# Kernel tuning notes

Hardware: AMD Instinct MI355X
Metric: run time of the kernel (lower is better)

The kernel has to match this reference:

```python
import jax, jax.numpy as jnp
import numpy as np


def setup_inputs() -> dict:
    key = jax.random.key(0)
    k1, k2, k3 = jax.random.split(key, 3)
    B, C, H, W, F, K = 8, 32, 64, 64, 64, 3
    x = jax.random.normal(k1, (B, C, H, W), dtype=jnp.float32)
    # per-weight rational (safe Pade [5/4]) coefficients: one activation per (f, a, b, c)
    num_coef = jax.random.normal(k2, (F, K, K, C, 6), dtype=jnp.float32) * 0.1
    den_coef = jax.random.normal(k3, (F, K, K, C, 4), dtype=jnp.float32) * 0.1
    return {"x": x, "num_coef": num_coef, "den_coef": den_coef}


def _rational(x, an, bd):
    """Safe Pade rational: P(x)/(1+|x*(b1+x*(b2+x*(b3+x*b4)))|).
    x: [B,H,W,K,K,C]; an: [K,K,C,6]; bd: [K,K,C,4] (broadcast over B,H,W)."""
    num = an[..., 5]
    for i in (4, 3, 2, 1, 0):  # Horner, ascending coeff order a0..a5
        num = num * x + an[..., i]
    q = bd[..., 3]
    for i in (2, 1, 0):
        q = q * x + bd[..., i]
    den = 1.0 + jnp.abs(q * x)
    return num / den


def reference(x, num_coef, den_coef):
    B, C, H, W = x.shape
    F, K = num_coef.shape[0], num_coef.shape[1]
    p = (K - 1) // 2
    xp = jnp.pad(x, ((0, 0), (0, 0), (p, p), (p, p)))  # zero pad H,W
    xp = jnp.transpose(xp, (0, 2, 3, 1))  # [B, H+2p, W+2p, C]
    # im2col patches: [B, H, W, K, K, C]
    patches = jnp.stack(
        [jnp.stack([xp[:, a:a + H, b:b + W, :] for b in range(K)], axis=3)
         for a in range(K)], axis=3)

    def per_filter(coefs):
        an, bd = coefs  # [K,K,C,6], [K,K,C,4]
        y = _rational(patches, an, bd)  # [B,H,W,K,K,C]
        return jnp.sum(y, axis=(3, 4, 5))  # [B,H,W]

    out = jax.lax.map(per_filter, (num_coef, den_coef))  # [F,B,H,W]
    return jnp.transpose(out, (1, 0, 2, 3))  # [B,F,H,W]
```

## Files before the change

### kernel.cpp

```cpp
#include <hip/hip_runtime.h>


typedef int   iv4  __attribute__((ext_vector_type(4)));
typedef short s8v  __attribute__((ext_vector_type(8)));
typedef float f16v __attribute__((ext_vector_type(16)));

#define Bb 8
#define Cc 32
#define Hh 64
#define Ww 64
#define Ff 64
#define PW 66
#define PPLANE (PW * PW)
#define NELEM  (Bb * Cc * PPLANE)
#define NTAP   288
#define ACOEF_N (NTAP * 4 * 64)

static __device__ __forceinline__ unsigned short f2bf(float f) {
    unsigned u = __builtin_bit_cast(unsigned, f);
    u += 0x7fffu + ((u >> 16) & 1u);
    return (unsigned short)(u >> 16);
}
static __device__ __forceinline__ float bf2f(unsigned short h) {
    unsigned u = ((unsigned)h) << 16;
    return __builtin_bit_cast(float, u);
}
static __device__ __forceinline__ int pack2(unsigned short a, unsigned short b) {
    return (int)((unsigned)a | ((unsigned)b << 16));
}

__global__ __launch_bounds__(256) void powers_kernel(
    const float* __restrict__ x, iv4* __restrict__ pw)
{
    int idx = (int)blockIdx.x * 256 + (int)threadIdx.x;
    int wp = idx % PW;
    int r1 = idx / PW;
    int hp = r1 % PW;
    int pl = r1 / PW;
    float v = 0.0f;
    if (hp >= 1 && hp <= Hh && wp >= 1 && wp <= Ww)
        v = x[((size_t)pl * Hh + (hp - 1)) * Ww + (wp - 1)];
    float p1 = v, p2 = v * v, p3 = p2 * v, p4 = p2 * p2, p5 = p4 * v;
    float pv[6] = {1.0f, p1, p2, p3, p4, p5};
    unsigned short hi[6], lo[6];
#pragma unroll
    for (int e = 0; e < 6; ++e) {
        hi[e] = f2bf(pv[e]);
        lo[e] = f2bf(pv[e] - bf2f(hi[e]));
    }
    iv4 r0, r1v;
    r0.x  = pack2(hi[0], hi[1]); r0.y  = pack2(hi[2], hi[3]);
    r0.z  = pack2(hi[4], hi[5]); r0.w  = pack2(lo[1], lo[2]);
    r1v.x = pack2(lo[3], lo[4]); r1v.y = pack2(lo[5], hi[1]);
    r1v.z = pack2(hi[2], hi[3]); r1v.w = pack2(hi[4], hi[5]);
    pw[idx]         = r0;
    pw[NELEM + idx] = r1v;
}

__global__ __launch_bounds__(256) void acoef_kernel(
    const float* __restrict__ ncf, const float* __restrict__ dcf,
    iv4* __restrict__ ac)
{
    int idx = (int)blockIdx.x * 256 + (int)threadIdx.x;
    int l = idx & 63, tile = (idx >> 6) & 3, t = idx >> 8;
    int m = l & 31, g = l >> 5;
    float cv[6];
    if (tile < 2) {
        int f = tile * 32 + m;
        const float* s = ncf + ((size_t)f * NTAP + t) * 6;
        cv[0] = s[0]; cv[1] = s[1]; cv[2] = s[2];
        cv[3] = s[3]; cv[4] = s[4]; cv[5] = s[5];
    } else {
        int f = (tile - 2) * 32 + m;
        const float* s = dcf + ((size_t)f * NTAP + t) * 4;
        cv[0] = 0.0f; cv[1] = s[0]; cv[2] = s[1];
        cv[3] = s[2]; cv[4] = s[3]; cv[5] = 0.0f;
    }
    unsigned short chi[6], clo[6];
#pragma unroll
    for (int e = 0; e < 6; ++e) {
        chi[e] = f2bf(cv[e]);
        clo[e] = f2bf(cv[e] - bf2f(chi[e]));
    }
    iv4 o;
    if (g == 0) {
        o.x = pack2(chi[0], chi[1]); o.y = pack2(chi[2], chi[3]);
        o.z = pack2(chi[4], chi[5]); o.w = pack2(chi[1], chi[2]);
    } else {
        o.x = pack2(chi[3], chi[4]); o.y = pack2(chi[5], clo[1]);
        o.z = pack2(clo[2], clo[3]); o.w = pack2(clo[4], clo[5]);
    }
    ac[idx] = o;
}

__global__ __launch_bounds__(256, 4) void kan_mfma_kernel(
    const iv4* __restrict__ pw, const iv4* __restrict__ ac,
    float* __restrict__ out)
{
    const int tid = threadIdx.x;
    const int l = tid & 63, v = tid >> 6, ln = l & 31, g = l >> 5;
    const int gb = (int)blockIdx.x;
    const int wh = gb & 1, h = (gb >> 1) & 63, bb = gb >> 7;
    const int w0 = wh << 5;

    __shared__ float red[4][64][33];

    f16v acc0, acc1, zf;
#pragma unroll
    for (int r = 0; r < 16; ++r) { acc0[r] = 0.0f; acc1[r] = 0.0f; zf[r] = 0.0f; }

    const iv4* __restrict__ pwg = pw + (size_t)g * NELEM;

    const int tEnd = v * 72 + 72;
    for (int t = v * 72; t < tEnd; ++t) {
        const int c = t & 31, k2 = t >> 5;
        const int dy = k2 / 3, dx = k2 - dy * 3;
        const int elem = ((bb * Cc + c) * PW + (h + dy)) * PW + (w0 + ln + dx);
        iv4 bl = pwg[elem];
        const iv4* ap = ac + (size_t)t * 256;
        iv4 A0 = ap[l], A1 = ap[64 + l], A2 = ap[128 + l], A3 = ap[192 + l];
        s8v bF = __builtin_bit_cast(s8v, bl);

        f16v D0 = __builtin_amdgcn_mfma_f32_32x32x16_bf16(
            __builtin_bit_cast(s8v, A0), bF, zf, 0, 0, 0);
        f16v D2 = __builtin_amdgcn_mfma_f32_32x32x16_bf16(
            __builtin_bit_cast(s8v, A2), bF, zf, 0, 0, 0);
#pragma unroll
        for (int r = 0; r < 16; ++r) {
            float dd = 1.0f + __builtin_fabsf(D2[r]);
            float rc = __builtin_amdgcn_rcpf(dd);
            acc0[r] = __builtin_fmaf(D0[r], rc, acc0[r]);
        }
        f16v D1 = __builtin_amdgcn_mfma_f32_32x32x16_bf16(
            __builtin_bit_cast(s8v, A1), bF, zf, 0, 0, 0);
        f16v D3 = __builtin_amdgcn_mfma_f32_32x32x16_bf16(
            __builtin_bit_cast(s8v, A3), bF, zf, 0, 0, 0);
#pragma unroll
        for (int r = 0; r < 16; ++r) {
            float dd = 1.0f + __builtin_fabsf(D3[r]);
            float rc = __builtin_amdgcn_rcpf(dd);
            acc1[r] = __builtin_fmaf(D1[r], rc, acc1[r]);
        }
    }

#pragma unroll
    for (int r = 0; r < 16; ++r) {
        red[v][l][r]      = acc0[r];
        red[v][l][16 + r] = acc1[r];
    }
    __syncthreads();

#pragma unroll
    for (int jj = 0; jj < 8; ++jj) {
        int j = v * 8 + jj;
        float s = red[0][l][j] + red[1][l][j] + red[2][l][j] + red[3][l][j];
        int tt = j >> 4, r = j & 15;
        int f = tt * 32 + (r & 3) + ((r >> 2) << 3) + ((l >> 5) << 2);
        out[(((size_t)bb * Ff + f) * Hh + h) * Ww + w0 + ln] = s;
    }
}

extern "C" void kernel_launch(void* const* d_in, const int* in_sizes, int n_in,
                              void* d_out, int out_size, void* d_ws, size_t ws_size,
                              hipStream_t stream) {
    const float* x   = (const float*)d_in[0];
    const float* ncf = (const float*)d_in[1];
    const float* dcf = (const float*)d_in[2];
    float* out = (float*)d_out;

    iv4* pw = (iv4*)d_ws;
    iv4* ac = pw + 2 * NELEM;

    powers_kernel<<<NELEM / 256, 256, 0, stream>>>(x, pw);
    acoef_kernel<<<NTAP, 256, 0, stream>>>(ncf, dcf, ac);
    kan_mfma_kernel<<<1024, 256, 0, stream>>>(pw, ac, out);
}
```

Before: 162.0 us.

## Merge prep kernels and split filter halves across 8 waves with prefetch

```diff
diff --git a/kernel.cpp b/kernel.cpp
--- a/kernel.cpp
+++ b/kernel.cpp
@@ -14,7 +14,7 @@
 #define PPLANE (PW * PW)
 #define NELEM  (Bb * Cc * PPLANE)
 #define NTAP   288
-#define ACOEF_N (NTAP * 4 * 64)
+#define PWBLK  (NELEM / 256)
 
 static __device__ __forceinline__ unsigned short f2bf(float f) {
     unsigned u = __builtin_bit_cast(unsigned, f);
@@ -29,133 +29,137 @@
     return (int)((unsigned)a | ((unsigned)b << 16));
 }
 
-__global__ __launch_bounds__(256) void powers_kernel(
-    const float* __restrict__ x, iv4* __restrict__ pw)
+__global__ __launch_bounds__(256) void prep_kernel(
+    const float* __restrict__ x,
+    const float* __restrict__ ncf, const float* __restrict__ dcf,
+    iv4* __restrict__ pw, iv4* __restrict__ ac)
 {
-    int idx = (int)blockIdx.x * 256 + (int)threadIdx.x;
-    int wp = idx % PW;
-    int r1 = idx / PW;
-    int hp = r1 % PW;
-    int pl = r1 / PW;
-    float v = 0.0f;
-    if (hp >= 1 && hp <= Hh && wp >= 1 && wp <= Ww)
-        v = x[((size_t)pl * Hh + (hp - 1)) * Ww + (wp - 1)];
-    float p1 = v, p2 = v * v, p3 = p2 * v, p4 = p2 * p2, p5 = p4 * v;
-    float pv[6] = {1.0f, p1, p2, p3, p4, p5};
-    unsigned short hi[6], lo[6];
+    if ((int)blockIdx.x < PWBLK) {
+        int idx = (int)blockIdx.x * 256 + (int)threadIdx.x;
+        int wp = idx % PW;
+        int r1 = idx / PW;
+        int hp = r1 % PW;
+        int pl = r1 / PW;
+        float v = 0.0f;
+        if (hp >= 1 && hp <= Hh && wp >= 1 && wp <= Ww)
+            v = x[((size_t)pl * Hh + (hp - 1)) * Ww + (wp - 1)];
+        float p2 = v * v, p3 = p2 * v, p4 = p2 * p2, p5 = p4 * v;
+        float pv[6] = {1.0f, v, p2, p3, p4, p5};
+        unsigned short hi[6], lo[6];
 #pragma unroll
-    for (int e = 0; e < 6; ++e) {
-        hi[e] = f2bf(pv[e]);
-        lo[e] = f2bf(pv[e] - bf2f(hi[e]));
+        for (int e = 0; e < 6; ++e) {
+            hi[e] = f2bf(pv[e]);
+            lo[e] = f2bf(pv[e] - bf2f(hi[e]));
+        }
+        iv4 r0, r1v;
+        r0.x  = pack2(hi[0], hi[1]); r0.y  = pack2(hi[2], hi[3]);
+        r0.z  = pack2(hi[4], hi[5]); r0.w  = pack2(lo[1], lo[2]);
+        r1v.x = pack2(lo[3], lo[4]); r1v.y = pack2(lo[5], hi[1]);
+        r1v.z = pack2(hi[2], hi[3]); r1v.w = pack2(hi[4], hi[5]);
+        pw[idx]         = r0;
+        pw[NELEM + idx] = r1v;
+    } else {
+        int idx = ((int)blockIdx.x - PWBLK) * 256 + (int)threadIdx.x;
+        int l = idx & 63, tile = (idx >> 6) & 3, t = idx >> 8;
+        int m = l & 31, g = l >> 5;
+        float cv[6];
+        if (tile < 2) {
+            int f = tile * 32 + m;
+            const float* s = ncf + ((size_t)f * NTAP + t) * 6;
+            cv[0] = s[0]; cv[1] = s[1]; cv[2] = s[2];
+            cv[3] = s[3]; cv[4] = s[4]; cv[5] = s[5];
+        } else {
+            int f = (tile - 2) * 32 + m;
+            const float* s = dcf + ((size_t)f * NTAP + t) * 4;
+            cv[0] = 0.0f; cv[1] = s[0]; cv[2] = s[1];
+            cv[3] = s[2]; cv[4] = s[3]; cv[5] = 0.0f;
+        }
+        unsigned short chi[6], clo[6];
+#pragma unroll
+        for (int e = 0; e < 6; ++e) {
+            chi[e] = f2bf(cv[e]);
+            clo[e] = f2bf(cv[e] - bf2f(chi[e]));
+        }
+        iv4 o;
+        if (g == 0) {
+            o.x = pack2(chi[0], chi[1]); o.y = pack2(chi[2], chi[3]);
+            o.z = pack2(chi[4], chi[5]); o.w = pack2(chi[1], chi[2]);
+        } else {
+            o.x = pack2(chi[3], chi[4]); o.y = pack2(chi[5], clo[1]);
+            o.z = pack2(clo[2], clo[3]); o.w = pack2(clo[4], clo[5]);
+        }
+        ac[idx] = o;
     }
-    iv4 r0, r1v;
-    r0.x  = pack2(hi[0], hi[1]); r0.y  = pack2(hi[2], hi[3]);
-    r0.z  = pack2(hi[4], hi[5]); r0.w  = pack2(lo[1], lo[2]);
-    r1v.x = pack2(lo[3], lo[4]); r1v.y = pack2(lo[5], hi[1]);
-    r1v.z = pack2(hi[2], hi[3]); r1v.w = pack2(hi[4], hi[5]);
-    pw[idx]         = r0;
-    pw[NELEM + idx] = r1v;
 }
 
-__global__ __launch_bounds__(256) void acoef_kernel(
-    const float* __restrict__ ncf, const float* __restrict__ dcf,
-    iv4* __restrict__ ac)
-{
-    int idx = (int)blockIdx.x * 256 + (int)threadIdx.x;
-    int l = idx & 63, tile = (idx >> 6) & 3, t = idx >> 8;
-    int m = l & 31, g = l >> 5;
-    float cv[6];
-    if (tile < 2) {
-        int f = tile * 32 + m;
-        const float* s = ncf + ((size_t)f * NTAP + t) * 6;
-        cv[0] = s[0]; cv[1] = s[1]; cv[2] = s[2];
-        cv[3] = s[3]; cv[4] = s[4]; cv[5] = s[5];
-    } else {
-        int f = (tile - 2) * 32 + m;
-        const float* s = dcf + ((size_t)f * NTAP + t) * 4;
-        cv[0] = 0.0f; cv[1] = s[0]; cv[2] = s[1];
-        cv[3] = s[2]; cv[4] = s[3]; cv[5] = 0.0f;
-    }
-    unsigned short chi[6], clo[6];
-#pragma unroll
-    for (int e = 0; e < 6; ++e) {
-        chi[e] = f2bf(cv[e]);
-        clo[e] = f2bf(cv[e] - bf2f(chi[e]));
-    }
-    iv4 o;
-    if (g == 0) {
-        o.x = pack2(chi[0], chi[1]); o.y = pack2(chi[2], chi[3]);
-        o.z = pack2(chi[4], chi[5]); o.w = pack2(chi[1], chi[2]);
-    } else {
-        o.x = pack2(chi[3], chi[4]); o.y = pack2(chi[5], clo[1]);
-        o.z = pack2(clo[2], clo[3]); o.w = pack2(clo[4], clo[5]);
-    }
-    ac[idx] = o;
-}
-
-__global__ __launch_bounds__(256, 4) void kan_mfma_kernel(
+__global__ __launch_bounds__(512, 4) void kan_mfma_kernel(
     const iv4* __restrict__ pw, const iv4* __restrict__ ac,
     float* __restrict__ out)
 {
     const int tid = threadIdx.x;
     const int l = tid & 63, v = tid >> 6, ln = l & 31, g = l >> 5;
+    const int p = v & 1, q = v >> 1;
     const int gb = (int)blockIdx.x;
     const int wh = gb & 1, h = (gb >> 1) & 63, bb = gb >> 7;
     const int w0 = wh << 5;
 
-    __shared__ float red[4][64][33];
+    __shared__ float red[4][2][64][17];
 
-    f16v acc0, acc1, zf;
+    f16v acc, zf;
 #pragma unroll
-    for (int r = 0; r < 16; ++r) { acc0[r] = 0.0f; acc1[r] = 0.0f; zf[r] = 0.0f; }
+    for (int r = 0; r < 16; ++r) { acc[r] = 0.0f; zf[r] = 0.0f; }
 
     const iv4* __restrict__ pwg = pw + (size_t)g * NELEM;
+    const int aoff = p * 64;
 
-    const int tEnd = v * 72 + 72;
-    for (int t = v * 72; t < tEnd; ++t) {
-        const int c = t & 31, k2 = t >> 5;
-        const int dy = k2 / 3, dx = k2 - dy * 3;
-        const int elem = ((bb * Cc + c) * PW + (h + dy)) * PW + (w0 + ln + dx);
-        iv4 bl = pwg[elem];
-        const iv4* ap = ac + (size_t)t * 256;
-        iv4 A0 = ap[l], A1 = ap[64 + l], A2 = ap[128 + l], A3 = ap[192 + l];
-        s8v bF = __builtin_bit_cast(s8v, bl);
+    const int t0 = q * 72, tEnd = t0 + 72;
 
-        f16v D0 = __builtin_amdgcn_mfma_f32_32x32x16_bf16(
-            __builtin_bit_cast(s8v, A0), bF, zf, 0, 0, 0);
-        f16v D2 = __builtin_amdgcn_mfma_f32_32x32x16_bf16(
-            __builtin_bit_cast(s8v, A2), bF, zf, 0, 0, 0);
+    int c = t0 & 31, k2 = t0 >> 5;
+    int dy = k2 / 3, dx = k2 - dy * 3;
+    int elem = ((bb * Cc + c) * PW + (h + dy)) * PW + (w0 + ln + dx);
+    iv4 blc = pwg[elem];
+    const iv4* ap = ac + (size_t)t0 * 256;
+    iv4 Anc = ap[aoff + l], Adc = ap[128 + aoff + l];
+
+#pragma unroll 1
+    for (int t = t0; t < tEnd; ++t) {
+        const int tn = (t + 1 < tEnd) ? t + 1 : t;
+        const int cn = tn & 31, k2n = tn >> 5;
+        const int dyn = k2n / 3, dxn = k2n - dyn * 3;
+        const int elemn = ((bb * Cc + cn) * PW + (h + dyn)) * PW + (w0 + ln + dxn);
+        iv4 bln = pwg[elemn];
+        const iv4* apn = ac + (size_t)tn * 256;
+        iv4 Ann = apn[aoff + l], Adn = apn[128 + aoff + l];
+
+        s8v bF = __builtin_bit_cast(s8v, blc);
+        f16v Dn = __builtin_amdgcn_mfma_f32_32x32x16_bf16(
+            __builtin_bit_cast(s8v, Anc), bF, zf, 0, 0, 0);
+        f16v Dd = __builtin_amdgcn_mfma_f32_32x32x16_bf16(
+            __builtin_bit_cast(s8v, Adc), bF, zf, 0, 0, 0);
+
 #pragma unroll
         for (int r = 0; r < 16; ++r) {
-            float dd = 1.0f + __builtin_fabsf(D2[r]);
+            float dd = 1.0f + __builtin_fabsf(Dd[r]);
             float rc = __builtin_amdgcn_rcpf(dd);
-            acc0[r] = __builtin_fmaf(D0[r], rc, acc0[r]);
+            acc[r] = __builtin_fmaf(Dn[r], rc, acc[r]);
         }
-        f16v D1 = __builtin_amdgcn_mfma_f32_32x32x16_bf16(
-            __builtin_bit_cast(s8v, A1), bF, zf, 0, 0, 0);
-        f16v D3 = __builtin_amdgcn_mfma_f32_32x32x16_bf16(
-            __builtin_bit_cast(s8v, A3), bF, zf, 0, 0, 0);
-#pragma unroll
-        for (int r = 0; r < 16; ++r) {
-            float dd = 1.0f + __builtin_fabsf(D3[r]);
-            float rc = __builtin_amdgcn_rcpf(dd);
-            acc1[r] = __builtin_fmaf(D1[r], rc, acc1[r]);
-        }
+
+        blc = bln; Anc = Ann; Adc = Adn;
     }
 
 #pragma unroll
-    for (int r = 0; r < 16; ++r) {
-        red[v][l][r]      = acc0[r];
-        red[v][l][16 + r] = acc1[r];
-    }
+    for (int r = 0; r < 16; ++r)
+        red[q][p][l][r] = acc[r];
     __syncthreads();
 
+    const int u = v;
+    const int p2 = u & 1;
 #pragma unroll
-    for (int jj = 0; jj < 8; ++jj) {
-        int j = v * 8 + jj;
-        float s = red[0][l][j] + red[1][l][j] + red[2][l][j] + red[3][l][j];
-        int tt = j >> 4, r = j & 15;
-        int f = tt * 32 + (r & 3) + ((r >> 2) << 3) + ((l >> 5) << 2);
+    for (int jj = 0; jj < 4; ++jj) {
+        int r = (u >> 1) * 4 + jj;
+        float s = red[0][p2][l][r] + red[1][p2][l][r]
+                + red[2][p2][l][r] + red[3][p2][l][r];
+        int f = p2 * 32 + (r & 3) + ((r >> 2) << 3) + ((l >> 5) << 2);
         out[(((size_t)bb * Ff + f) * Hh + h) * Ww + w0 + ln] = s;
     }
 }
@@ -171,7 +175,6 @@
     iv4* pw = (iv4*)d_ws;
     iv4* ac = pw + 2 * NELEM;
 
-    powers_kernel<<<NELEM / 256, 256, 0, stream>>>(x, pw);
-    acoef_kernel<<<NTAP, 256, 0, stream>>>(ncf, dcf, ac);
-    kan_mfma_kernel<<<1024, 256, 0, stream>>>(pw, ac, out);
+    prep_kernel<<<PWBLK + NTAP, 256, 0, stream>>>(x, ncf, dcf, pw, ac);
+    kan_mfma_kernel<<<1024, 512, 0, stream>>>(pw, ac, out);
 }
```

After: 161.6 us. About the same (-0.3%).

## Switch bf16 hi/lo split to single fp16 MFMA and merge prep kernels

Applied to the files above, without the earlier changes.

```diff
diff --git a/kernel.cpp b/kernel.cpp
--- a/kernel.cpp
+++ b/kernel.cpp
@@ -14,83 +14,63 @@
 #define PPLANE (PW * PW)
 #define NELEM  (Bb * Cc * PPLANE)
 #define NTAP   288
-#define ACOEF_N (NTAP * 4 * 64)
+#define PWBLK  (NELEM / 256)
 
-static __device__ __forceinline__ unsigned short f2bf(float f) {
-    unsigned u = __builtin_bit_cast(unsigned, f);
-    u += 0x7fffu + ((u >> 16) & 1u);
-    return (unsigned short)(u >> 16);
-}
-static __device__ __forceinline__ float bf2f(unsigned short h) {
-    unsigned u = ((unsigned)h) << 16;
-    return __builtin_bit_cast(float, u);
+static __device__ __forceinline__ unsigned short f2h(float f) {
+    return __builtin_bit_cast(unsigned short, (_Float16)f);
 }
 static __device__ __forceinline__ int pack2(unsigned short a, unsigned short b) {
     return (int)((unsigned)a | ((unsigned)b << 16));
 }
-
-__global__ __launch_bounds__(256) void powers_kernel(
-    const float* __restrict__ x, iv4* __restrict__ pw)
-{
-    int idx = (int)blockIdx.x * 256 + (int)threadIdx.x;
-    int wp = idx % PW;
-    int r1 = idx / PW;
-    int hp = r1 % PW;
-    int pl = r1 / PW;
-    float v = 0.0f;
-    if (hp >= 1 && hp <= Hh && wp >= 1 && wp <= Ww)
-        v = x[((size_t)pl * Hh + (hp - 1)) * Ww + (wp - 1)];
-    float p1 = v, p2 = v * v, p3 = p2 * v, p4 = p2 * p2, p5 = p4 * v;
-    float pv[6] = {1.0f, p1, p2, p3, p4, p5};
-    unsigned short hi[6], lo[6];
-#pragma unroll
-    for (int e = 0; e < 6; ++e) {
-        hi[e] = f2bf(pv[e]);
-        lo[e] = f2bf(pv[e] - bf2f(hi[e]));
-    }
-    iv4 r0, r1v;
-    r0.x  = pack2(hi[0], hi[1]); r0.y  = pack2(hi[2], hi[3]);
-    r0.z  = pack2(hi[4], hi[5]); r0.w  = pack2(lo[1], lo[2]);
-    r1v.x = pack2(lo[3], lo[4]); r1v.y = pack2(lo[5], hi[1]);
-    r1v.z = pack2(hi[2], hi[3]); r1v.w = pack2(hi[4], hi[5]);
-    pw[idx]         = r0;
-    pw[NELEM + idx] = r1v;
+static __device__ __forceinline__ iv4 ld16(const char* p) {
+    return *(const iv4* __restrict__)p;
 }
 
-__global__ __launch_bounds__(256) void acoef_kernel(
+__global__ __launch_bounds__(256) void prep_kernel(
+    const float* __restrict__ x,
     const float* __restrict__ ncf, const float* __restrict__ dcf,
-    iv4* __restrict__ ac)
+    iv4* __restrict__ pw, iv4* __restrict__ ac)
 {
-    int idx = (int)blockIdx.x * 256 + (int)threadIdx.x;
-    int l = idx & 63, tile = (idx >> 6) & 3, t = idx >> 8;
-    int m = l & 31, g = l >> 5;
-    float cv[6];
-    if (tile < 2) {
-        int f = tile * 32 + m;
-        const float* s = ncf + ((size_t)f * NTAP + t) * 6;
-        cv[0] = s[0]; cv[1] = s[1]; cv[2] = s[2];
-        cv[3] = s[3]; cv[4] = s[4]; cv[5] = s[5];
+    if ((int)blockIdx.x < PWBLK) {
+        int idx = (int)blockIdx.x * 256 + (int)threadIdx.x;
+        if (idx == 0) { iv4 z = {0, 0, 0, 0}; pw[NELEM] = z; }
+        int wp = idx % PW;
+        int r1 = idx / PW;
+        int hp = r1 % PW;
+        int pl = r1 / PW;
+        float v = 0.0f;
+        if (hp >= 1 && hp <= Hh && wp >= 1 && wp <= Ww)
+            v = x[((size_t)pl * Hh + (hp - 1)) * Ww + (wp - 1)];
+        float p2 = v * v, p3 = p2 * v, p4 = p2 * p2, p5 = p4 * v;
+        iv4 r0;
+        r0.x = pack2((unsigned short)0x3C00, f2h(v));
+        r0.y = pack2(f2h(p2), f2h(p3));
+        r0.z = pack2(f2h(p4), f2h(p5));
+        r0.w = 0;
+        pw[idx] = r0;
     } else {
-        int f = (tile - 2) * 32 + m;
-        const float* s = dcf + ((size_t)f * NTAP + t) * 4;
-        cv[0] = 0.0f; cv[1] = s[0]; cv[2] = s[1];
-        cv[3] = s[2]; cv[4] = s[3]; cv[5] = 0.0f;
+        int idx = ((int)blockIdx.x - PWBLK) * 256 + (int)threadIdx.x;
+        int l = idx & 63, tile = (idx >> 6) & 3, t = idx >> 8;
+        int m = l & 31;
+        float cv[6];
+        if (tile < 2) {
+            int f = tile * 32 + m;
+            const float* s = ncf + ((size_t)f * NTAP + t) * 6;
+            cv[0] = s[0]; cv[1] = s[1]; cv[2] = s[2];
+            cv[3] = s[3]; cv[4] = s[4]; cv[5] = s[5];
+        } else {
+            int f = (tile - 2) * 32 + m;
+            const float* s = dcf + ((size_t)f * NTAP + t) * 4;
+            cv[0] = 0.0f; cv[1] = s[0]; cv[2] = s[1];
+            cv[3] = s[2]; cv[4] = s[3]; cv[5] = 0.0f;
+        }
+        iv4 o;
+        o.x = pack2(f2h(cv[0]), f2h(cv[1]));
+        o.y = pack2(f2h(cv[2]), f2h(cv[3]));
+        o.z = pack2(f2h(cv[4]), f2h(cv[5]));
+        o.w = 0;
+        ac[idx] = o;
     }
-    unsigned short chi[6], clo[6];
-#pragma unroll
-    for (int e = 0; e < 6; ++e) {
-        chi[e] = f2bf(cv[e]);
-        clo[e] = f2bf(cv[e] - bf2f(chi[e]));
-    }
-    iv4 o;
-    if (g == 0) {
-        o.x = pack2(chi[0], chi[1]); o.y = pack2(chi[2], chi[3]);
-        o.z = pack2(chi[4], chi[5]); o.w = pack2(chi[1], chi[2]);
-    } else {
-        o.x = pack2(chi[3], chi[4]); o.y = pack2(chi[5], clo[1]);
-        o.z = pack2(clo[2], clo[3]); o.w = pack2(clo[4], clo[5]);
-    }
-    ac[idx] = o;
 }
 
 __global__ __launch_bounds__(256, 4) void kan_mfma_kernel(
@@ -109,21 +89,24 @@
 #pragma unroll
     for (int r = 0; r < 16; ++r) { acc0[r] = 0.0f; acc1[r] = 0.0f; zf[r] = 0.0f; }
 
-    const iv4* __restrict__ pwg = pw + (size_t)g * NELEM;
+    const char* __restrict__ pwc = (const char*)pw;
+    const unsigned baseB = (g == 0) ? 0u : (unsigned)NELEM * 16u;
+    const unsigned mE    = (g == 0) ? 0xFFFFFFFFu : 0u;
 
     const int tEnd = v * 72 + 72;
+#pragma unroll 1
     for (int t = v * 72; t < tEnd; ++t) {
         const int c = t & 31, k2 = t >> 5;
         const int dy = k2 / 3, dx = k2 - dy * 3;
         const int elem = ((bb * Cc + c) * PW + (h + dy)) * PW + (w0 + ln + dx);
-        iv4 bl = pwg[elem];
+        iv4 bl = ld16(pwc + (baseB + (((unsigned)(elem * 16)) & mE)));
         const iv4* ap = ac + (size_t)t * 256;
         iv4 A0 = ap[l], A1 = ap[64 + l], A2 = ap[128 + l], A3 = ap[192 + l];
         s8v bF = __builtin_bit_cast(s8v, bl);
 
-        f16v D0 = __builtin_amdgcn_mfma_f32_32x32x16_bf16(
+        f16v D0 = __builtin_amdgcn_mfma_f32_32x32x16_f16(
             __builtin_bit_cast(s8v, A0), bF, zf, 0, 0, 0);
-        f16v D2 = __builtin_amdgcn_mfma_f32_32x32x16_bf16(
+        f16v D2 = __builtin_amdgcn_mfma_f32_32x32x16_f16(
             __builtin_bit_cast(s8v, A2), bF, zf, 0, 0, 0);
 #pragma unroll
         for (int r = 0; r < 16; ++r) {
@@ -131,9 +114,9 @@
             float rc = __builtin_amdgcn_rcpf(dd);
             acc0[r] = __builtin_fmaf(D0[r], rc, acc0[r]);
         }
-        f16v D1 = __builtin_amdgcn_mfma_f32_32x32x16_bf16(
+        f16v D1 = __builtin_amdgcn_mfma_f32_32x32x16_f16(
             __builtin_bit_cast(s8v, A1), bF, zf, 0, 0, 0);
-        f16v D3 = __builtin_amdgcn_mfma_f32_32x32x16_bf16(
+        f16v D3 = __builtin_amdgcn_mfma_f32_32x32x16_f16(
             __builtin_bit_cast(s8v, A3), bF, zf, 0, 0, 0);
 #pragma unroll
         for (int r = 0; r < 16; ++r) {
@@ -169,9 +152,8 @@
     float* out = (float*)d_out;
 
     iv4* pw = (iv4*)d_ws;
-    iv4* ac = pw + 2 * NELEM;
+    iv4* ac = pw + NELEM + 1;
 
-    powers_kernel<<<NELEM / 256, 256, 0, stream>>>(x, pw);
-    acoef_kernel<<<NTAP, 256, 0, stream>>>(ncf, dcf, ac);
+    prep_kernel<<<PWBLK + NTAP, 256, 0, stream>>>(x, ncf, dcf, pw, ac);
     kan_mfma_kernel<<<1024, 256, 0, stream>>>(pw, ac, out);
 }
```

Measured after the change: 154.1 us. -4.9%, faster.
